# Optimization experiments

Hardware: AMD Instinct MI355X
Metric: run time of the kernel (lower is better)

## Reference

```python
import jax, jax.numpy as jnp
import numpy as np

N_NODES = 100000
N_EDGES = 640000
D_IN = 128
D_OUT = 128
D_HID = 128  # assumed MLP hidden width (repo MLP not shown; standard 2-layer GIN MLP)


def setup_inputs() -> dict:
    key = jax.random.key(0)
    k = jax.random.split(key, 8)
    x = jax.random.normal(k[0], (N_NODES, D_IN), dtype=jnp.float32)
    edge_index = jax.random.randint(k[1], (2, N_EDGES), 0, N_NODES, dtype=jnp.int64)
    edge_attr = jax.random.normal(k[2], (N_EDGES, D_IN), dtype=jnp.float32)
    # learned params
    eps = jnp.zeros((), dtype=jnp.float32)  # train_eps=True, init 0
    s1 = 1.0 / np.sqrt(D_IN)
    s2 = 1.0 / np.sqrt(D_HID)
    W1 = jax.random.uniform(k[3], (D_IN, D_HID), jnp.float32, -s1, s1)
    b1 = jax.random.uniform(k[4], (D_HID,), jnp.float32, -s1, s1)
    W2 = jax.random.uniform(k[5], (D_HID, D_OUT), jnp.float32, -s2, s2)
    b2 = jax.random.uniform(k[6], (D_OUT,), jnp.float32, -s2, s2)
    return {"x": x, "edge_index": edge_index, "edge_attr": edge_attr,
            "eps": eps, "W1": W1, "b1": b1, "W2": W2, "b2": b2}


def reference(x, edge_index, edge_attr, eps, W1, b1, W2, b2):
    src = edge_index[0]  # source nodes j
    dst = edge_index[1]  # target nodes i
    # message: ReLU(x_j + edge_attr)  -- [E, D_IN]
    msg = jax.nn.relu(x[src] + edge_attr)
    # scatter-sum aggregation to target nodes -- [N, D_IN]
    aggr = jax.ops.segment_sum(msg, dst, num_segments=N_NODES)
    # GINE update: (1 + eps) * x_i + aggr, then MLP (dropout=0.0 -> identity)
    h = (1.0 + eps) * x + aggr
    h = jax.nn.relu(h @ W1 + b1)
    out = h @ W2 + b2
    return out
```

## Files before the change

### kernel.cpp

```cpp
#include <hip/hip_runtime.h>

constexpr int NN = 100000;
constexpr int NE = 640000;
constexpr int D  = 128;
constexpr int NB = (NN + 255) / 256;

typedef __attribute__((ext_vector_type(8))) short bf16x8;
typedef __attribute__((ext_vector_type(4))) float f32x4;

__device__ __forceinline__ short f2bf(float f) {
    union { float f; unsigned u; } v; v.f = f;
    unsigned r = v.u + 0x7FFF + ((v.u >> 16) & 1);
    return (short)(r >> 16);
}
__device__ __forceinline__ float bf2f(short h) {
    union { unsigned u; float f; } v;
    v.u = ((unsigned)(unsigned short)h) << 16;
    return v.f;
}

__global__ __launch_bounds__(256) void k_zero(int* __restrict__ cnt) {
    int i = blockIdx.x * 256 + threadIdx.x;
    if (i < NN) cnt[i] = 0;
}

__global__ __launch_bounds__(256) void k_hist(const int* __restrict__ dst,
                                              int* __restrict__ cnt) {
    int e = blockIdx.x * 256 + threadIdx.x;
    if (e < NE) atomicAdd(&cnt[dst[e]], 1);
}

__global__ __launch_bounds__(256) void k_bsum(const int* __restrict__ cnt,
                                              int* __restrict__ bsum) {
    int i = blockIdx.x * 256 + threadIdx.x;
    int v = (i < NN) ? cnt[i] : 0;
#pragma unroll
    for (int s = 32; s; s >>= 1) v += __shfl_down(v, s, 64);
    __shared__ int w[4];
    if ((threadIdx.x & 63) == 0) w[threadIdx.x >> 6] = v;
    __syncthreads();
    if (threadIdx.x == 0) bsum[blockIdx.x] = w[0] + w[1] + w[2] + w[3];
}

__global__ __launch_bounds__(512) void k_scan_bsum(const int* __restrict__ bsum,
                                                   int* __restrict__ bboff) {
    int t = threadIdx.x, lane = t & 63;
    int v = (t < NB) ? bsum[t] : 0;
    int incl = v;
#pragma unroll
    for (int s = 1; s < 64; s <<= 1) {
        int u = __shfl_up(incl, s, 64);
        if (lane >= s) incl += u;
    }
    __shared__ int wt[8], wp[8];
    if (lane == 63) wt[t >> 6] = incl;
    __syncthreads();
    if (t == 0) { int run = 0; for (int i = 0; i < 8; ++i) { wp[i] = run; run += wt[i]; } }
    __syncthreads();
    if (t < NB) bboff[t] = incl - v + wp[t >> 6];
}

__global__ __launch_bounds__(256) void k_scan_final(const int* __restrict__ cnt,
                                                    const int* __restrict__ bboff,
                                                    int* __restrict__ off,
                                                    int* __restrict__ cur) {
    int b = blockIdx.x, t = threadIdx.x, lane = t & 63;
    int i = b * 256 + t;
    int v = (i < NN) ? cnt[i] : 0;
    int incl = v;
#pragma unroll
    for (int s = 1; s < 64; s <<= 1) {
        int u = __shfl_up(incl, s, 64);
        if (lane >= s) incl += u;
    }
    __shared__ int wt[4], wp[4];
    if (lane == 63) wt[t >> 6] = incl;
    __syncthreads();
    if (t == 0) { int run = 0; for (int q = 0; q < 4; ++q) { wp[q] = run; run += wt[q]; } }
    __syncthreads();
    int excl = incl - v + wp[t >> 6] + bboff[b];
    if (i < NN) { off[i] = excl; cur[i] = excl; }
    if (i == 0) off[NN] = NE;
}

__global__ __launch_bounds__(256) void k_pos(const int* __restrict__ dst,
                                             int* __restrict__ cur,
                                             int* __restrict__ pos) {
    int e = blockIdx.x * 256 + threadIdx.x;
    if (e < NE) pos[e] = atomicAdd(&cur[dst[e]], 1);
}

__global__ __launch_bounds__(256) void k_wsplit(const float* __restrict__ W,
                                                short* __restrict__ Whi,
                                                short* __restrict__ Wlo) {
    for (int idx = blockIdx.x * 256 + threadIdx.x; idx < D * D; idx += gridDim.x * 256) {
        int n = idx >> 7, k = idx & 127;
        float w = W[k * D + n];
        short hi = f2bf(w);
        Whi[idx] = hi;
        Wlo[idx] = f2bf(w - bf2f(hi));
    }
}

__global__ __launch_bounds__(256) void k_msg(const float* __restrict__ x,
                                             const int* __restrict__ src,
                                             const float* __restrict__ ea,
                                             const int* __restrict__ pos,
                                             unsigned short* __restrict__ mbuf) {
    unsigned gid = blockIdx.x * 256 + threadIdx.x;
    unsigned e = gid >> 4;
    unsigned c = gid & 15;
    const int s = src[e];
    const int p = pos[e];
    const float* eap = ea + (size_t)e * D + c * 8;
    const float* xp  = x  + (size_t)s * D + c * 8;
    float4 a0 = reinterpret_cast<const float4*>(xp)[0];
    float4 a1 = reinterpret_cast<const float4*>(xp)[1];
    float4 b0 = reinterpret_cast<const float4*>(eap)[0];
    float4 b1 = reinterpret_cast<const float4*>(eap)[1];
    float m[8] = {a0.x + b0.x, a0.y + b0.y, a0.z + b0.z, a0.w + b0.w,
                  a1.x + b1.x, a1.y + b1.y, a1.z + b1.z, a1.w + b1.w};
    bf16x8 o;
#pragma unroll
    for (int i = 0; i < 8; ++i) o[i] = f2bf(fmaxf(m[i], 0.0f));
    *reinterpret_cast<bf16x8*>(mbuf + (size_t)p * D + c * 8) = o;
}

__global__ __launch_bounds__(256) void k_agg2(const float* __restrict__ x,
                                              const unsigned short* __restrict__ mbuf,
                                              const int* __restrict__ off,
                                              const float* __restrict__ eps,
                                              float* __restrict__ h) {
    int wave = threadIdx.x >> 6;
    int lane = threadIdx.x & 63;
    int n = blockIdx.x * 4 + wave;
    if (n >= NN) return;
    int j0 = off[n], j1 = off[n + 1];
    const int lo2 = lane * 2;
    float accx = 0.0f, accy = 0.0f;

    for (int j = j0; j < j1; j += 4) {
        ushort2 mv[4];
#pragma unroll
        for (int q = 0; q < 4; ++q) {
            int jj = j + q; jj = (jj < j1) ? jj : (j1 - 1);
            mv[q] = *reinterpret_cast<const ushort2*>(mbuf + (size_t)jj * D + lo2);
        }
#pragma unroll
        for (int q = 0; q < 4; ++q) {
            bool ok = (j + q) < j1;
            accx += ok ? bf2f((short)mv[q].x) : 0.0f;
            accy += ok ? bf2f((short)mv[q].y) : 0.0f;
        }
    }
    float sc = 1.0f + eps[0];
    float2 xx = *reinterpret_cast<const float2*>(x + (size_t)n * D + lo2);
    float2 o;
    o.x = fmaf(sc, xx.x, accx);
    o.y = fmaf(sc, xx.y, accy);
    *reinterpret_cast<float2*>(h + (size_t)n * D + lo2) = o;
}

__global__ __launch_bounds__(256) void k_mlp2(const float* __restrict__ A,
                                              const short* __restrict__ W1h,
                                              const short* __restrict__ W1l,
                                              const short* __restrict__ W2h,
                                              const short* __restrict__ W2l,
                                              const float* __restrict__ b1,
                                              const float* __restrict__ b2,
                                              float* __restrict__ out) {
    __shared__ float G[4][32][D];

    const int wave = threadIdx.x >> 6;
    const int lane = threadIdx.x & 63;
    const int r = lane & 15;
    const int g = lane >> 4;

    const long rb = (long)blockIdx.x * 128 + wave * 32;

    f32x4 acc1[2][8];
#pragma unroll
    for (int mt = 0; mt < 2; ++mt)
#pragma unroll
        for (int nt = 0; nt < 8; ++nt) {
            acc1[mt][nt].x = 0.f; acc1[mt][nt].y = 0.f;
            acc1[mt][nt].z = 0.f; acc1[mt][nt].w = 0.f;
        }

#pragma unroll
    for (int kc = 0; kc < 4; ++kc) {
        const int k0 = kc * 32;
        bf16x8 ahi[2], alo[2];
#pragma unroll
        for (int mt = 0; mt < 2; ++mt) {
            long row = rb + mt * 16 + r;
            row = (row < NN) ? row : (NN - 1);
            const float* ap = A + row * D + k0 + g * 8;
            float4 v0 = reinterpret_cast<const float4*>(ap)[0];
            float4 v1 = reinterpret_cast<const float4*>(ap)[1];
            float vals[8] = {v0.x, v0.y, v0.z, v0.w, v1.x, v1.y, v1.z, v1.w};
#pragma unroll
            for (int i = 0; i < 8; ++i) {
                short hb = f2bf(vals[i]);
                ahi[mt][i] = hb;
                alo[mt][i] = f2bf(vals[i] - bf2f(hb));
            }
        }
#pragma unroll
        for (int nt = 0; nt < 8; ++nt) {
            const int wb = (nt * 16 + r) * D + k0 + g * 8;
            bf16x8 whi = *reinterpret_cast<const bf16x8*>(&W1h[wb]);
            bf16x8 wlo = *reinterpret_cast<const bf16x8*>(&W1l[wb]);
#pragma unroll
            for (int mt = 0; mt < 2; ++mt) {
                acc1[mt][nt] = __builtin_amdgcn_mfma_f32_16x16x32_bf16(ahi[mt], whi, acc1[mt][nt], 0, 0, 0);
                acc1[mt][nt] = __builtin_amdgcn_mfma_f32_16x16x32_bf16(ahi[mt], wlo, acc1[mt][nt], 0, 0, 0);
                acc1[mt][nt] = __builtin_amdgcn_mfma_f32_16x16x32_bf16(alo[mt], whi, acc1[mt][nt], 0, 0, 0);
            }
        }
    }

#pragma unroll
    for (int nt = 0; nt < 8; ++nt) {
        const int col = nt * 16 + r;
        const float bb = b1[col];
#pragma unroll
        for (int mt = 0; mt < 2; ++mt) {
#pragma unroll
            for (int q = 0; q < 4; ++q) {
                float v = fmaxf(acc1[mt][nt][q] + bb, 0.0f);
                G[wave][mt * 16 + g * 4 + q][col] = v;
            }
        }
    }
    __syncthreads();

    f32x4 acc2[2][8];
#pragma unroll
    for (int mt = 0; mt < 2; ++mt)
#pragma unroll
        for (int nt = 0; nt < 8; ++nt) {
            acc2[mt][nt].x = 0.f; acc2[mt][nt].y = 0.f;
            acc2[mt][nt].z = 0.f; acc2[mt][nt].w = 0.f;
        }

#pragma unroll
    for (int kc = 0; kc < 4; ++kc) {
        const int k0 = kc * 32;
        bf16x8 ahi[2], alo[2];
#pragma unroll
        for (int mt = 0; mt < 2; ++mt) {
            const float* gp = &G[wave][mt * 16 + r][k0 + g * 8];
            float4 v0 = reinterpret_cast<const float4*>(gp)[0];
            float4 v1 = reinterpret_cast<const float4*>(gp)[1];
            float vals[8] = {v0.x, v0.y, v0.z, v0.w, v1.x, v1.y, v1.z, v1.w};
#pragma unroll
            for (int i = 0; i < 8; ++i) {
                short hb = f2bf(vals[i]);
                ahi[mt][i] = hb;
                alo[mt][i] = f2bf(vals[i] - bf2f(hb));
            }
        }
#pragma unroll
        for (int nt = 0; nt < 8; ++nt) {
            const int wb = (nt * 16 + r) * D + k0 + g * 8;
            bf16x8 whi = *reinterpret_cast<const bf16x8*>(&W2h[wb]);
            bf16x8 wlo = *reinterpret_cast<const bf16x8*>(&W2l[wb]);
#pragma unroll
            for (int mt = 0; mt < 2; ++mt) {
                acc2[mt][nt] = __builtin_amdgcn_mfma_f32_16x16x32_bf16(ahi[mt], whi, acc2[mt][nt], 0, 0, 0);
                acc2[mt][nt] = __builtin_amdgcn_mfma_f32_16x16x32_bf16(ahi[mt], wlo, acc2[mt][nt], 0, 0, 0);
                acc2[mt][nt] = __builtin_amdgcn_mfma_f32_16x16x32_bf16(alo[mt], whi, acc2[mt][nt], 0, 0, 0);
            }
        }
    }

#pragma unroll
    for (int nt = 0; nt < 8; ++nt) {
        const int col = nt * 16 + r;
        const float bb = b2[col];
#pragma unroll
        for (int mt = 0; mt < 2; ++mt) {
#pragma unroll
            for (int q = 0; q < 4; ++q) {
                long row = rb + mt * 16 + g * 4 + q;
                if (row < NN) out[row * D + col] = acc2[mt][nt][q] + bb;
            }
        }
    }
}

extern "C" void kernel_launch(void* const* d_in, const int* in_sizes, int n_in,
                              void* d_out, int out_size, void* d_ws, size_t ws_size,
                              hipStream_t stream) {
    const float* x   = (const float*)d_in[0];
    const int*   ei  = (const int*)d_in[1];
    const float* ea  = (const float*)d_in[2];
    const float* eps = (const float*)d_in[3];
    const float* W1  = (const float*)d_in[4];
    const float* b1  = (const float*)d_in[5];
    const float* W2  = (const float*)d_in[6];
    const float* b2  = (const float*)d_in[7];
    float* out = (float*)d_out;

    const int* src = ei;
    const int* dst = ei + NE;

    int* base  = (int*)d_ws;
    int* cnt   = base;
    int* off   = cnt + NN;
    int* cur   = off + NN + 1;
    int* bsum  = cur + NN;
    int* bboff = bsum + NB;
    int* pos   = bboff + NB;
    size_t mb_off = ((size_t)(3 * NN + 1 + 2 * NB + NE) + 63) & ~(size_t)63;
    unsigned short* mbuf = (unsigned short*)(base + mb_off);
    short* wsp = (short*)(mbuf + (size_t)NE * D);
    short* W1h = wsp;
    short* W1l = W1h + D * D;
    short* W2h = W1l + D * D;
    short* W2l = W2h + D * D;

    k_wsplit    <<<32,               256, 0, stream>>>(W1, W1h, W1l);
    k_wsplit    <<<32,               256, 0, stream>>>(W2, W2h, W2l);
    k_zero      <<<NB,               256, 0, stream>>>(cnt);
    k_hist      <<<(NE + 255) / 256, 256, 0, stream>>>(dst, cnt);
    k_bsum      <<<NB,               256, 0, stream>>>(cnt, bsum);
    k_scan_bsum <<<1,                512, 0, stream>>>(bsum, bboff);
    k_scan_final<<<NB,               256, 0, stream>>>(cnt, bboff, off, cur);
    k_pos       <<<(NE + 255) / 256, 256, 0, stream>>>(dst, cur, pos);

    k_msg <<<NE * 16 / 256, 256, 0, stream>>>(x, src, ea, pos, mbuf);
    k_agg2<<<(NN + 3) / 4, 256, 0, stream>>>(x, mbuf, off, eps, out);
    k_mlp2<<<(NN + 127) / 128, 256, 0, stream>>>(out, W1h, W1l, W2h, W2l, b1, b2, out);
}
```

Before: 323.0 us.

## Replace per-node CSR sort with coarse 128-node bins and LDS atomic aggregation

Edges are now bucketed by destination into 782 bins of 128 nodes instead of sorted by node. A small LDS histogram plus a single-block scan replaces the multi-kernel per-node count/scan/position pipeline. k_msg takes its slot with an atomic on the bin cursor and records the local destination. Each aggregation block accumulates its bin into a 64KB LDS tile with float atomics, then adds the scaled x. This removes several launches and the per-node offset arrays, at the cost of LDS atomic contention, 64KB of LDS per block (low occupancy), and a non-deterministic summation order.

After: 908.7 us. +181.3%, slower.

```diff
diff --git a/kernel.cpp b/kernel.cpp
--- a/kernel.cpp
+++ b/kernel.cpp
@@ -3,7 +3,8 @@
 constexpr int NN = 100000;
 constexpr int NE = 640000;
 constexpr int D  = 128;
-constexpr int NB = (NN + 255) / 256;
+constexpr int BINB = 128;
+constexpr int KB = (NN + BINB - 1) / BINB;
 
 typedef __attribute__((ext_vector_type(8))) short bf16x8;
 typedef __attribute__((ext_vector_type(4))) float f32x4;
@@ -19,75 +20,44 @@
     return v.f;
 }
 
-__global__ __launch_bounds__(256) void k_zero(int* __restrict__ cnt) {
+__global__ __launch_bounds__(256) void k_bzero(int* __restrict__ cnt) {
     int i = blockIdx.x * 256 + threadIdx.x;
-    if (i < NN) cnt[i] = 0;
-}
-
-__global__ __launch_bounds__(256) void k_hist(const int* __restrict__ dst,
-                                              int* __restrict__ cnt) {
-    int e = blockIdx.x * 256 + threadIdx.x;
-    if (e < NE) atomicAdd(&cnt[dst[e]], 1);
-}
-
-__global__ __launch_bounds__(256) void k_bsum(const int* __restrict__ cnt,
-                                              int* __restrict__ bsum) {
-    int i = blockIdx.x * 256 + threadIdx.x;
-    int v = (i < NN) ? cnt[i] : 0;
-#pragma unroll
-    for (int s = 32; s; s >>= 1) v += __shfl_down(v, s, 64);
-    __shared__ int w[4];
-    if ((threadIdx.x & 63) == 0) w[threadIdx.x >> 6] = v;
-    __syncthreads();
-    if (threadIdx.x == 0) bsum[blockIdx.x] = w[0] + w[1] + w[2] + w[3];
-}
-
-__global__ __launch_bounds__(512) void k_scan_bsum(const int* __restrict__ bsum,
-                                                   int* __restrict__ bboff) {
+    if (i < KB) cnt[i] = 0;
+}
+
+__global__ __launch_bounds__(256) void k_bhist(const int* __restrict__ dst,
+                                               int* __restrict__ cnt) {
+    __shared__ int lh[KB];
+    for (int i = threadIdx.x; i < KB; i += 256) lh[i] = 0;
+    __syncthreads();
+    for (int e = blockIdx.x * 256 + threadIdx.x; e < NE; e += gridDim.x * 256)
+        atomicAdd(&lh[dst[e] >> 7], 1);
+    __syncthreads();
+    for (int i = threadIdx.x; i < KB; i += 256) {
+        int v = lh[i];
+        if (v) atomicAdd(&cnt[i], v);
+    }
+}
+
+__global__ __launch_bounds__(1024) void k_bscan(const int* __restrict__ cnt,
+                                                int* __restrict__ binoff,
+                                                int* __restrict__ cur) {
     int t = threadIdx.x, lane = t & 63;
-    int v = (t < NB) ? bsum[t] : 0;
+    int v = (t < KB) ? cnt[t] : 0;
     int incl = v;
 #pragma unroll
     for (int s = 1; s < 64; s <<= 1) {
         int u = __shfl_up(incl, s, 64);
         if (lane >= s) incl += u;
     }
-    __shared__ int wt[8], wp[8];
+    __shared__ int wt[16], wp[16];
     if (lane == 63) wt[t >> 6] = incl;
     __syncthreads();
-    if (t == 0) { int run = 0; for (int i = 0; i < 8; ++i) { wp[i] = run; run += wt[i]; } }
-    __syncthreads();
-    if (t < NB) bboff[t] = incl - v + wp[t >> 6];
-}
-
-__global__ __launch_bounds__(256) void k_scan_final(const int* __restrict__ cnt,
-                                                    const int* __restrict__ bboff,
-                                                    int* __restrict__ off,
-                                                    int* __restrict__ cur) {
-    int b = blockIdx.x, t = threadIdx.x, lane = t & 63;
-    int i = b * 256 + t;
-    int v = (i < NN) ? cnt[i] : 0;
-    int incl = v;
-#pragma unroll
-    for (int s = 1; s < 64; s <<= 1) {
-        int u = __shfl_up(incl, s, 64);
-        if (lane >= s) incl += u;
-    }
-    __shared__ int wt[4], wp[4];
-    if (lane == 63) wt[t >> 6] = incl;
-    __syncthreads();
-    if (t == 0) { int run = 0; for (int q = 0; q < 4; ++q) { wp[q] = run; run += wt[q]; } }
-    __syncthreads();
-    int excl = incl - v + wp[t >> 6] + bboff[b];
-    if (i < NN) { off[i] = excl; cur[i] = excl; }
-    if (i == 0) off[NN] = NE;
-}
-
-__global__ __launch_bounds__(256) void k_pos(const int* __restrict__ dst,
-                                             int* __restrict__ cur,
-                                             int* __restrict__ pos) {
-    int e = blockIdx.x * 256 + threadIdx.x;
-    if (e < NE) pos[e] = atomicAdd(&cur[dst[e]], 1);
+    if (t == 0) { int run = 0; for (int i = 0; i < 16; ++i) { wp[i] = run; run += wt[i]; } }
+    __syncthreads();
+    int excl = incl - v + wp[t >> 6];
+    if (t < KB) { binoff[t] = excl; cur[t] = excl; }
+    if (t == 0) binoff[KB] = NE;
 }
 
 __global__ __launch_bounds__(256) void k_wsplit(const float* __restrict__ W,
@@ -104,16 +74,26 @@
 
 __global__ __launch_bounds__(256) void k_msg(const float* __restrict__ x,
                                              const int* __restrict__ src,
+                                             const int* __restrict__ dst,
                                              const float* __restrict__ ea,
-                                             const int* __restrict__ pos,
+                                             int* __restrict__ cur,
+                                             unsigned short* __restrict__ mdst,
                                              unsigned short* __restrict__ mbuf) {
     unsigned gid = blockIdx.x * 256 + threadIdx.x;
     unsigned e = gid >> 4;
     unsigned c = gid & 15;
+    const int lane = threadIdx.x & 63;
     const int s = src[e];
-    const int p = pos[e];
+    const int d = dst[e];
+    int slot = 0;
+    if (c == 0) {
+        slot = atomicAdd(&cur[d >> 7], 1);
+        mdst[slot] = (unsigned short)(d & (BINB - 1));
+    }
+    slot = __shfl(slot, lane & 48, 64);
+
+    const float* xp  = x  + (size_t)s * D + c * 8;
     const float* eap = ea + (size_t)e * D + c * 8;
-    const float* xp  = x  + (size_t)s * D + c * 8;
     float4 a0 = reinterpret_cast<const float4*>(xp)[0];
     float4 a1 = reinterpret_cast<const float4*>(xp)[1];
     float4 b0 = reinterpret_cast<const float4*>(eap)[0];
@@ -123,42 +103,69 @@
     bf16x8 o;
 #pragma unroll
     for (int i = 0; i < 8; ++i) o[i] = f2bf(fmaxf(m[i], 0.0f));
-    *reinterpret_cast<bf16x8*>(mbuf + (size_t)p * D + c * 8) = o;
-}
-
-__global__ __launch_bounds__(256) void k_agg2(const float* __restrict__ x,
+    *reinterpret_cast<bf16x8*>(mbuf + (size_t)slot * D + c * 8) = o;
+}
+
+__global__ __launch_bounds__(256) void k_bagg(const float* __restrict__ x,
                                               const unsigned short* __restrict__ mbuf,
-                                              const int* __restrict__ off,
+                                              const unsigned short* __restrict__ mdst,
+                                              const int* __restrict__ binoff,
                                               const float* __restrict__ eps,
                                               float* __restrict__ h) {
-    int wave = threadIdx.x >> 6;
-    int lane = threadIdx.x & 63;
-    int n = blockIdx.x * 4 + wave;
-    if (n >= NN) return;
-    int j0 = off[n], j1 = off[n + 1];
+    __shared__ float acc[BINB * D];
+    float4* a4 = reinterpret_cast<float4*>(acc);
+    for (int i = threadIdx.x; i < BINB * D / 4; i += 256) {
+        float4 z; z.x = 0.f; z.y = 0.f; z.z = 0.f; z.w = 0.f;
+        a4[i] = z;
+    }
+    __syncthreads();
+
+    const int b = blockIdx.x;
+    const int wave = threadIdx.x >> 6;
+    const int lane = threadIdx.x & 63;
+    const int j0 = binoff[b], j1 = binoff[b + 1];
     const int lo2 = lane * 2;
-    float accx = 0.0f, accy = 0.0f;
-
-    for (int j = j0; j < j1; j += 4) {
-        ushort2 mv[4];
-#pragma unroll
-        for (int q = 0; q < 4; ++q) {
-            int jj = j + q; jj = (jj < j1) ? jj : (j1 - 1);
-            mv[q] = *reinterpret_cast<const ushort2*>(mbuf + (size_t)jj * D + lo2);
-        }
-#pragma unroll
-        for (int q = 0; q < 4; ++q) {
-            bool ok = (j + q) < j1;
-            accx += ok ? bf2f((short)mv[q].x) : 0.0f;
-            accy += ok ? bf2f((short)mv[q].y) : 0.0f;
-        }
-    }
-    float sc = 1.0f + eps[0];
-    float2 xx = *reinterpret_cast<const float2*>(x + (size_t)n * D + lo2);
-    float2 o;
-    o.x = fmaf(sc, xx.x, accx);
-    o.y = fmaf(sc, xx.y, accy);
-    *reinterpret_cast<float2*>(h + (size_t)n * D + lo2) = o;
+
+    const int base = j0 + wave;
+    const int nmine = (j1 - base + 3) >> 2;
+    for (int i0 = 0; i0 < nmine; i0 += 8) {
+        ushort2 mv[8];
+        int ld[8];
+        bool ok[8];
+#pragma unroll
+        for (int q = 0; q < 8; ++q) {
+            int j = base + 4 * (i0 + q);
+            ok[q] = j < j1;
+            int jc = ok[q] ? j : (j1 - 1);
+            mv[q] = *reinterpret_cast<const ushort2*>(mbuf + (size_t)jc * D + lo2);
+            ld[q] = mdst[jc];
+        }
+#pragma unroll
+        for (int q = 0; q < 8; ++q) {
+            if (ok[q]) {
+                atomicAdd(&acc[ld[q] * D + lo2],     bf2f((short)mv[q].x));
+                atomicAdd(&acc[ld[q] * D + lo2 + 1], bf2f((short)mv[q].y));
+            }
+        }
+    }
+    __syncthreads();
+
+    const float sc = 1.0f + eps[0];
+    const long n0 = (long)b * BINB;
+    for (int v = threadIdx.x; v < BINB * (D / 4); v += 256) {
+        int row = v >> 5, q = v & 31;
+        long node = n0 + row;
+        if (node < NN) {
+            float4 a = a4[v];
+            float4 xx = reinterpret_cast<const float4*>(x)[node * (D / 4) + q];
+            float4 o;
+            o.x = fmaf(sc, xx.x, a.x);
+            o.y = fmaf(sc, xx.y, a.y);
+            o.z = fmaf(sc, xx.z, a.z);
+            o.w = fmaf(sc, xx.w, a.w);
+            reinterpret_cast<float4*>(h)[node * (D / 4) + q] = o;
+        }
+    }
 }
 
 __global__ __launch_bounds__(256) void k_mlp2(const float* __restrict__ A,
@@ -306,31 +313,25 @@
     const int* src = ei;
     const int* dst = ei + NE;
 
-    int* base  = (int*)d_ws;
-    int* cnt   = base;
-    int* off   = cnt + NN;
-    int* cur   = off + NN + 1;
-    int* bsum  = cur + NN;
-    int* bboff = bsum + NB;
-    int* pos   = bboff + NB;
-    size_t mb_off = ((size_t)(3 * NN + 1 + 2 * NB + NE) + 63) & ~(size_t)63;
-    unsigned short* mbuf = (unsigned short*)(base + mb_off);
+    int* cnt    = (int*)d_ws;
+    int* binoff = cnt + KB;
+    int* cur    = binoff + KB + 1;
+    unsigned short* mdst = (unsigned short*)(cur + KB);
+    size_t mb_off = (((size_t)(3 * KB + 1) * 4 + (size_t)NE * 2) + 255) & ~(size_t)255;
+    unsigned short* mbuf = (unsigned short*)((char*)d_ws + mb_off);
     short* wsp = (short*)(mbuf + (size_t)NE * D);
     short* W1h = wsp;
     short* W1l = W1h + D * D;
     short* W2h = W1l + D * D;
     short* W2l = W2h + D * D;
 
-    k_wsplit    <<<32,               256, 0, stream>>>(W1, W1h, W1l);
-    k_wsplit    <<<32,               256, 0, stream>>>(W2, W2h, W2l);
-    k_zero      <<<NB,               256, 0, stream>>>(cnt);
-    k_hist      <<<(NE + 255) / 256, 256, 0, stream>>>(dst, cnt);
-    k_bsum      <<<NB,               256, 0, stream>>>(cnt, bsum);
-    k_scan_bsum <<<1,                512, 0, stream>>>(bsum, bboff);
-    k_scan_final<<<NB,               256, 0, stream>>>(cnt, bboff, off, cur);
-    k_pos       <<<(NE + 255) / 256, 256, 0, stream>>>(dst, cur, pos);
-
-    k_msg <<<NE * 16 / 256, 256, 0, stream>>>(x, src, ea, pos, mbuf);
-    k_agg2<<<(NN + 3) / 4, 256, 0, stream>>>(x, mbuf, off, eps, out);
+    k_wsplit<<<32, 256, 0, stream>>>(W1, W1h, W1l);
+    k_wsplit<<<32, 256, 0, stream>>>(W2, W2h, W2l);
+    k_bzero <<<(KB + 255) / 256, 256, 0, stream>>>(cnt);
+    k_bhist <<<256, 256, 0, stream>>>(dst, cnt);
+    k_bscan <<<1, 1024, 0, stream>>>(cnt, binoff, cur);
+
+    k_msg<<<NE * 16 / 256, 256, 0, stream>>>(x, src, dst, ea, cur, mdst, mbuf);
+    k_bagg<<<KB, 256, 0, stream>>>(x, mbuf, mdst, binoff, eps, out);
     k_mlp2<<<(NN + 127) / 128, 256, 0, stream>>>(out, W1h, W1l, W2h, W2l, b1, b2, out);
 }
```
